# Performance work log

Measured on AMD Instinct MI355X. Metric: run time of the kernel, lower is better.

The kernel has to match this reference:

```python
import jax, jax.numpy as jnp
import numpy as np

N = 50000          # nodes
E = 1000000        # edges
EMB = 64           # emb_dim
L = 3              # num_layer
B = 250            # graphs (200 nodes each)
XF, EF = 7, 5      # node / edge feature dims
BN_EPS = 1e-5


def setup_inputs() -> dict:
    key = jax.random.key(0)
    ks = jax.random.split(key, 16)
    x = jax.random.normal(ks[0], (N, XF), dtype=jnp.float32)
    edge_attr = jax.random.normal(ks[1], (E, EF), dtype=jnp.float32)
    edge_index = jax.random.randint(ks[2], (2, E), 0, N, dtype=jnp.int32)
    # 250 contiguous graphs of 200 nodes: last node index of each graph
    last_idx = jnp.arange(1, B + 1, dtype=jnp.int32) * (N // B) - 1
    s = 0.05
    xW = jax.random.normal(ks[3], (XF, EMB), dtype=jnp.float32) * s
    xb = jnp.zeros((EMB,), dtype=jnp.float32)
    eW = jax.random.normal(ks[4], (L, EF, EMB), dtype=jnp.float32) * s
    eb = jnp.zeros((L, EMB), dtype=jnp.float32)
    W1 = jax.random.normal(ks[5], (L, EMB, 2 * EMB), dtype=jnp.float32) * s
    b1 = jnp.zeros((L, 2 * EMB), dtype=jnp.float32)
    W2 = jax.random.normal(ks[6], (L, 2 * EMB, EMB), dtype=jnp.float32) * s
    b2 = jnp.zeros((L, EMB), dtype=jnp.float32)
    gamma = jnp.ones((L, EMB), dtype=jnp.float32)
    beta = jnp.zeros((L, EMB), dtype=jnp.float32)
    return {"x": x, "edge_attr": edge_attr, "edge_index": edge_index,
            "last_idx": last_idx, "xW": xW, "xb": xb, "eW": eW, "eb": eb,
            "W1": W1, "b1": b1, "W2": W2, "b2": b2,
            "gamma": gamma, "beta": beta}


def _gnn_forward(x, edge_attr, edge_index, last_idx, xW, xb, eW, eb, W1, b1, W2, b2, gamma, beta):
    n = x.shape[0]
    # self-loop edge attrs: first column = 8, rest 0
    self_attr = jnp.zeros((n, EF), dtype=edge_attr.dtype).at[:, 0].set(8.0)
    ea = jnp.concatenate([edge_attr, self_attr], axis=0)          # [E+N, EF]
    loop = jnp.arange(n, dtype=edge_index.dtype)
    src = jnp.concatenate([edge_index[0], loop])                  # x_j indices
    dst = jnp.concatenate([edge_index[1], loop])                  # aggregation targets

    h = x @ xW + xb                                               # [N, EMB]
    for l in range(L):
        e = ea @ eW[l] + eb[l]                                    # [E+N, EMB]
        msg = h[src] + e                                          # gather + combine
        agg = jax.ops.segment_sum(msg, dst, num_segments=n)       # scatter-add
        h2 = jax.nn.relu(agg @ W1[l] + b1[l]) @ W2[l] + b2[l]     # GIN MLP
        mean = jnp.mean(h2, axis=0)
        var = jnp.mean(jnp.square(h2 - mean), axis=0)             # biased, like torch BN
        hn = (h2 - mean) * jax.lax.rsqrt(var + BN_EPS) * gamma[l] + beta[l]
        h = jax.nn.elu(hn) if l < L - 1 else hn                   # drop_ratio = 0
    return h[last_idx]                                            # super-node reps [B, EMB]


def reference(x, edge_attr, edge_index, last_idx, xW, xb, eW, eb, W1, b1, W2, b2, gamma, beta):
    return _gnn_forward(x, edge_attr, edge_index, last_idx, xW, xb, eW, eb, W1, b1, W2, b2, gamma, beta)
```

## Files before the change

kernel.cpp:

```cpp
#include <hip/hip_runtime.h>

#define N_NODES 50000
#define N_EDGES 1000000
#define EMB     64
#define HID     128
#define NLAYER  3
#define NGRAPH  250
#define XFD     7
#define EFD     5
#define BN_EPS  1e-5f

#define NBKT  196
#define CHKE  4096
#define NCHK  245
#define CNTM  (NBKT * NCHK)
#define NB2   ((CNTM + 255) / 256)

__device__ __forceinline__ void atomAddF(float* p, float v) {
    __hip_atomic_fetch_add(p, v, __ATOMIC_RELAXED, __HIP_MEMORY_SCOPE_AGENT);
}

__global__ void k_input(const float* __restrict__ x, const float* __restrict__ xW,
                        const float* __restrict__ xb, float* __restrict__ h) {
    int gid = blockIdx.x * 256 + threadIdx.x;
    if (gid >= N_NODES * EMB) return;
    int n = gid >> 6, f = gid & 63;
    float acc = xb[f];
#pragma unroll
    for (int k = 0; k < XFD; ++k) acc = fmaf(x[n * XFD + k], xW[k * EMB + f], acc);
    h[gid] = acc;
}

__global__ __launch_bounds__(256) void k_binA(const int* __restrict__ dst,
                                              int* __restrict__ cntmat) {
    __shared__ int hist[NBKT];
    int tid = threadIdx.x, c = blockIdx.x;
    for (int i = tid; i < NBKT; i += 256) hist[i] = 0;
    __syncthreads();
    int e0 = c * CHKE, e1 = min(e0 + CHKE, N_EDGES);
    for (int i = e0 + tid; i < e1; i += 256) atomicAdd(&hist[dst[i] >> 8], 1);
    __syncthreads();
    for (int b = tid; b < NBKT; b += 256) cntmat[b * NCHK + c] = hist[b];
}

__global__ __launch_bounds__(256) void k_gscanA(const int* __restrict__ in, int n,
                                                int* __restrict__ bsum) {
    int tid = threadIdx.x, lane = tid & 63, wid = tid >> 6;
    int i = blockIdx.x * 256 + tid;
    int v = (i < n) ? in[i] : 0;
#pragma unroll
    for (int off = 32; off; off >>= 1) v += __shfl_down(v, off);
    __shared__ int ws[4];
    if (lane == 0) ws[wid] = v;
    __syncthreads();
    if (tid == 0) bsum[blockIdx.x] = ws[0] + ws[1] + ws[2] + ws[3];
}

__global__ __launch_bounds__(256) void k_gscanB(const int* __restrict__ bsum, int nb,
                                                int* __restrict__ boff) {
    int tid = threadIdx.x, lane = tid & 63, wid = tid >> 6;
    int v = (tid < nb) ? bsum[tid] : 0;
    int x = v;
#pragma unroll
    for (int off = 1; off < 64; off <<= 1) {
        int y = __shfl_up(x, off);
        if (lane >= off) x += y;
    }
    __shared__ int wtot[4];
    if (lane == 63) wtot[wid] = x;
    __syncthreads();
    int woff = 0;
    for (int w = 0; w < wid; ++w) woff += wtot[w];
    if (tid < nb) boff[tid] = woff + x - v;
}

__global__ __launch_bounds__(256) void k_gscanC(const int* __restrict__ in, int n,
                                                const int* __restrict__ boff,
                                                int* __restrict__ out) {
    int tid = threadIdx.x, lane = tid & 63, wid = tid >> 6;
    int i = blockIdx.x * 256 + tid;
    int v = (i < n) ? in[i] : 0;
    int x = v;
#pragma unroll
    for (int off = 1; off < 64; off <<= 1) {
        int y = __shfl_up(x, off);
        if (lane >= off) x += y;
    }
    __shared__ int wtot[4];
    if (lane == 63) wtot[wid] = x;
    __syncthreads();
    int woff = boff[blockIdx.x];
    for (int w = 0; w < wid; ++w) woff += wtot[w];
    if (i < n) out[i] = woff + x - v;
}

__global__ __launch_bounds__(256) void k_binC(const int* __restrict__ src,
                                              const int* __restrict__ dst,
                                              const int* __restrict__ off2,
                                              int4* __restrict__ buf) {
    __shared__ int cur[NBKT];
    int tid = threadIdx.x, c = blockIdx.x;
    for (int b = tid; b < NBKT; b += 256) cur[b] = off2[b * NCHK + c];
    __syncthreads();
    int e0 = c * CHKE, e1 = min(e0 + CHKE, N_EDGES);
    for (int i = e0 + tid; i < e1; i += 256) {
        int d = dst[i];
        int b = d >> 8;
        int p = atomicAdd(&cur[b], 1);
        buf[p] = make_int4(src[i], i, d, 0);
    }
}

__global__ __launch_bounds__(256) void k_binD(const int4* __restrict__ buf,
                                              const int* __restrict__ off2,
                                              const float* __restrict__ ea,
                                              int* __restrict__ csr,
                                              int* __restrict__ rowstart,
                                              float* __restrict__ aggE) {
    __shared__ int hist[256];
    __shared__ int cur[256];
    __shared__ float accL[256 * EFD];
    __shared__ int wtot[4];
    int tid = threadIdx.x, b = blockIdx.x;
    int bstart = off2[b * NCHK];
    int bend = (b + 1 < NBKT) ? off2[(b + 1) * NCHK] : N_EDGES;
    hist[tid] = 0;
    for (int i = tid; i < 256 * EFD; i += 256) accL[i] = 0.f;
    __syncthreads();
    for (int j = bstart + tid; j < bend; j += 256) atomicAdd(&hist[buf[j].z & 255], 1);
    __syncthreads();
    int lane = tid & 63, wid = tid >> 6;
    int v = hist[tid], x = v;
#pragma unroll
    for (int off = 1; off < 64; off <<= 1) {
        int y = __shfl_up(x, off);
        if (lane >= off) x += y;
    }
    if (lane == 63) wtot[wid] = x;
    __syncthreads();
    int woff = 0;
    for (int w = 0; w < wid; ++w) woff += wtot[w];
    int ex = woff + x - v;
    cur[tid] = ex;
    int node = b * 256 + tid;
    if (node < N_NODES) rowstart[node] = bstart + ex;
    if (b == NBKT - 1 && tid == 255) rowstart[N_NODES] = N_EDGES;
    __syncthreads();
    for (int j = bstart + tid; j < bend; j += 256) {
        int4 t = buf[j];
        int local = t.z & 255;
        int p = atomicAdd(&cur[local], 1);
        csr[bstart + p] = t.x;
        const float* pe = ea + (size_t)t.y * EFD;
        atomicAdd(&accL[local * EFD + 0], pe[0]);
        atomicAdd(&accL[local * EFD + 1], pe[1]);
        atomicAdd(&accL[local * EFD + 2], pe[2]);
        atomicAdd(&accL[local * EFD + 3], pe[3]);
        atomicAdd(&accL[local * EFD + 4], pe[4]);
    }
    __syncthreads();
    int validN = min(256, N_NODES - b * 256);
    for (int i = tid; i < validN * EFD; i += 256)
        aggE[(size_t)b * 256 * EFD + i] = accL[i];
}

__global__ __launch_bounds__(256) void k_agg(const float* __restrict__ h,
                                             float* __restrict__ agg,
                                             const int* __restrict__ rowstart,
                                             const int* __restrict__ csr,
                                             const float* __restrict__ aggE,
                                             const float* __restrict__ eWl,
                                             const float* __restrict__ ebl) {
    int wid = (blockIdx.x * 256 + threadIdx.x) >> 6;
    int lane = threadIdx.x & 63;
    if (wid >= N_NODES) return;
    int n = wid;
    int lg = lane >> 4, lq = lane & 15;
    const float4* h4 = (const float4*)h;
    int j0 = rowstart[n], j1 = rowstart[n + 1];
    float4 acc = make_float4(0.f, 0.f, 0.f, 0.f);
    int j = j0;
    while (j < j1) {
        int take = j1 - j;
        if (take > 64) take = 64;
        int myid = (lane < take) ? csr[j + lane] : 0;
        int nt = (take + 3) >> 2;
        int t = 0;
        for (; t + 4 <= nt; t += 4) {
            int e0 = t * 4 + lg, e1 = e0 + 4, e2 = e0 + 8, e3 = e0 + 12;
            int s0 = __shfl(myid, e0), s1 = __shfl(myid, e1),
                s2 = __shfl(myid, e2), s3 = __shfl(myid, e3);
            float4 v0 = h4[(size_t)s0 * 16 + lq];
            float4 v1 = h4[(size_t)s1 * 16 + lq];
            float4 v2 = h4[(size_t)s2 * 16 + lq];
            float4 v3 = h4[(size_t)s3 * 16 + lq];
            if (e0 < take) { acc.x += v0.x; acc.y += v0.y; acc.z += v0.z; acc.w += v0.w; }
            if (e1 < take) { acc.x += v1.x; acc.y += v1.y; acc.z += v1.z; acc.w += v1.w; }
            if (e2 < take) { acc.x += v2.x; acc.y += v2.y; acc.z += v2.z; acc.w += v2.w; }
            if (e3 < take) { acc.x += v3.x; acc.y += v3.y; acc.z += v3.z; acc.w += v3.w; }
        }
        for (; t < nt; ++t) {
            int e = t * 4 + lg;
            int s = __shfl(myid, e);
            float4 v = h4[(size_t)s * 16 + lq];
            if (e < take) { acc.x += v.x; acc.y += v.y; acc.z += v.z; acc.w += v.w; }
        }
        j += take;
    }
    acc.x += __shfl_xor(acc.x, 16); acc.y += __shfl_xor(acc.y, 16);
    acc.z += __shfl_xor(acc.z, 16); acc.w += __shfl_xor(acc.w, 16);
    acc.x += __shfl_xor(acc.x, 32); acc.y += __shfl_xor(acc.y, 32);
    acc.z += __shfl_xor(acc.z, 32); acc.w += __shfl_xor(acc.w, 32);
    const float4* eW4 = (const float4*)eWl;
    float4 ew0 = eW4[lq], ew1 = eW4[16 + lq], ew2 = eW4[32 + lq],
           ew3 = eW4[48 + lq], ew4 = eW4[64 + lq];
    float4 eb4 = ((const float4*)ebl)[lq];
    float a0 = aggE[n * 5 + 0], a1 = aggE[n * 5 + 1], a2 = aggE[n * 5 + 2],
          a3 = aggE[n * 5 + 3], a4 = aggE[n * 5 + 4];
    float c0 = a0 + 8.f;
    float ce = (float)(j1 - j0) + 1.f;
    float4 bb = h4[(size_t)n * 16 + lq];
    bb.x = fmaf(c0, ew0.x, bb.x); bb.y = fmaf(c0, ew0.y, bb.y);
    bb.z = fmaf(c0, ew0.z, bb.z); bb.w = fmaf(c0, ew0.w, bb.w);
    bb.x = fmaf(a1, ew1.x, bb.x); bb.y = fmaf(a1, ew1.y, bb.y);
    bb.z = fmaf(a1, ew1.z, bb.z); bb.w = fmaf(a1, ew1.w, bb.w);
    bb.x = fmaf(a2, ew2.x, bb.x); bb.y = fmaf(a2, ew2.y, bb.y);
    bb.z = fmaf(a2, ew2.z, bb.z); bb.w = fmaf(a2, ew2.w, bb.w);
    bb.x = fmaf(a3, ew3.x, bb.x); bb.y = fmaf(a3, ew3.y, bb.y);
    bb.z = fmaf(a3, ew3.z, bb.z); bb.w = fmaf(a3, ew3.w, bb.w);
    bb.x = fmaf(a4, ew4.x, bb.x); bb.y = fmaf(a4, ew4.y, bb.y);
    bb.z = fmaf(a4, ew4.z, bb.z); bb.w = fmaf(a4, ew4.w, bb.w);
    bb.x = fmaf(ce, eb4.x, bb.x); bb.y = fmaf(ce, eb4.y, bb.y);
    bb.z = fmaf(ce, eb4.z, bb.z); bb.w = fmaf(ce, eb4.w, bb.w);
    if (lg == 0) {
        ((float4*)agg)[(size_t)n * 16 + lq] =
            make_float4(acc.x + bb.x, acc.y + bb.y, acc.z + bb.z, acc.w + bb.w);
    }
}

__global__ __launch_bounds__(256) void k_mlp1(const float* __restrict__ agg,
                                              float* __restrict__ hidden,
                                              const float* __restrict__ W1l,
                                              const float* __restrict__ b1l) {
    __shared__ float w1s[64 * 128];
    __shared__ float as[32 * 68];
    __shared__ float b1s[128];
    int tid = threadIdx.x;
    int n0 = blockIdx.x * 32;
    const float4* wg = (const float4*)W1l;
    float4* wsh = (float4*)w1s;
#pragma unroll
    for (int i = 0; i < 8; ++i) wsh[tid + i * 256] = wg[tid + i * 256];
    if (tid < 128) b1s[tid] = b1l[tid];
    const float4* ag4 = (const float4*)agg;
#pragma unroll
    for (int i = 0; i < 2; ++i) {
        int idx = tid + i * 256;
        int m = idx >> 4, kq = idx & 15;
        int nn = n0 + m;
        float4 v = make_float4(0.f, 0.f, 0.f, 0.f);
        if (nn < N_NODES) v = ag4[nn * 16 + kq];
        *(float4*)&as[m * 68 + kq * 4] = v;
    }
    __syncthreads();
    int j0 = (tid & 31) * 4;
    int m0 = (tid >> 5) * 4;
    float acc[4][4] = {};
#pragma unroll 8
    for (int k = 0; k < 64; ++k) {
        float4 w = *(const float4*)&w1s[k * 128 + j0];
        float a0 = as[(m0 + 0) * 68 + k];
        float a1 = as[(m0 + 1) * 68 + k];
        float a2 = as[(m0 + 2) * 68 + k];
        float a3 = as[(m0 + 3) * 68 + k];
        acc[0][0] = fmaf(a0, w.x, acc[0][0]); acc[0][1] = fmaf(a0, w.y, acc[0][1]);
        acc[0][2] = fmaf(a0, w.z, acc[0][2]); acc[0][3] = fmaf(a0, w.w, acc[0][3]);
        acc[1][0] = fmaf(a1, w.x, acc[1][0]); acc[1][1] = fmaf(a1, w.y, acc[1][1]);
        acc[1][2] = fmaf(a1, w.z, acc[1][2]); acc[1][3] = fmaf(a1, w.w, acc[1][3]);
        acc[2][0] = fmaf(a2, w.x, acc[2][0]); acc[2][1] = fmaf(a2, w.y, acc[2][1]);
        acc[2][2] = fmaf(a2, w.z, acc[2][2]); acc[2][3] = fmaf(a2, w.w, acc[2][3]);
        acc[3][0] = fmaf(a3, w.x, acc[3][0]); acc[3][1] = fmaf(a3, w.y, acc[3][1]);
        acc[3][2] = fmaf(a3, w.z, acc[3][2]); acc[3][3] = fmaf(a3, w.w, acc[3][3]);
    }
#pragma unroll
    for (int a = 0; a < 4; ++a) {
        int nn = n0 + m0 + a;
        if (nn < N_NODES) {
            float4 o;
            o.x = fmaxf(acc[a][0] + b1s[j0 + 0], 0.f);
            o.y = fmaxf(acc[a][1] + b1s[j0 + 1], 0.f);
            o.z = fmaxf(acc[a][2] + b1s[j0 + 2], 0.f);
            o.w = fmaxf(acc[a][3] + b1s[j0 + 3], 0.f);
            *(float4*)&hidden[nn * HID + j0] = o;
        }
    }
}

__global__ __launch_bounds__(256) void k_mlp2(const float* __restrict__ hidden,
                                              float* __restrict__ h2,
                                              const float* __restrict__ W2l,
                                              const float* __restrict__ b2l,
                                              float* __restrict__ stats) {
    __shared__ float w2s[128 * 64];
    __shared__ float hs[64 * 132];
    __shared__ float b2s[64];
    int tid = threadIdx.x;
    int n0 = blockIdx.x * 64;
    const float4* wg = (const float4*)W2l;
    float4* wsh = (float4*)w2s;
#pragma unroll
    for (int i = 0; i < 8; ++i) wsh[tid + i * 256] = wg[tid + i * 256];
    if (tid < 64) b2s[tid] = b2l[tid];
    const float4* hg4 = (const float4*)hidden;
#pragma unroll
    for (int i = 0; i < 8; ++i) {
        int idx = tid + i * 256;
        int m = idx >> 5, kq = idx & 31;
        int nn = n0 + m;
        float4 v = make_float4(0.f, 0.f, 0.f, 0.f);
        if (nn < N_NODES) v = hg4[nn * 32 + kq];
        *(float4*)&hs[m * 132 + kq * 4] = v;
    }
    __syncthreads();
    int f0 = (tid & 15) * 4;
    int m0 = (tid >> 4) * 4;
    float acc[4][4] = {};
#pragma unroll 8
    for (int k = 0; k < 128; ++k) {
        float4 w = *(const float4*)&w2s[k * 64 + f0];
        float a0 = hs[(m0 + 0) * 132 + k];
        float a1 = hs[(m0 + 1) * 132 + k];
        float a2 = hs[(m0 + 2) * 132 + k];
        float a3 = hs[(m0 + 3) * 132 + k];
        acc[0][0] = fmaf(a0, w.x, acc[0][0]); acc[0][1] = fmaf(a0, w.y, acc[0][1]);
        acc[0][2] = fmaf(a0, w.z, acc[0][2]); acc[0][3] = fmaf(a0, w.w, acc[0][3]);
        acc[1][0] = fmaf(a1, w.x, acc[1][0]); acc[1][1] = fmaf(a1, w.y, acc[1][1]);
        acc[1][2] = fmaf(a1, w.z, acc[1][2]); acc[1][3] = fmaf(a1, w.w, acc[1][3]);
        acc[2][0] = fmaf(a2, w.x, acc[2][0]); acc[2][1] = fmaf(a2, w.y, acc[2][1]);
        acc[2][2] = fmaf(a2, w.z, acc[2][2]); acc[2][3] = fmaf(a2, w.w, acc[2][3]);
        acc[3][0] = fmaf(a3, w.x, acc[3][0]); acc[3][1] = fmaf(a3, w.y, acc[3][1]);
        acc[3][2] = fmaf(a3, w.z, acc[3][2]); acc[3][3] = fmaf(a3, w.w, acc[3][3]);
    }
    float sf[4] = {0.f, 0.f, 0.f, 0.f}, qf[4] = {0.f, 0.f, 0.f, 0.f};
#pragma unroll
    for (int a = 0; a < 4; ++a) {
        int nn = n0 + m0 + a;
        if (nn < N_NODES) {
            float v0 = acc[a][0] + b2s[f0 + 0];
            float v1 = acc[a][1] + b2s[f0 + 1];
            float v2 = acc[a][2] + b2s[f0 + 2];
            float v3 = acc[a][3] + b2s[f0 + 3];
            *(float4*)&h2[nn * EMB + f0] = make_float4(v0, v1, v2, v3);
            sf[0] += v0; sf[1] += v1; sf[2] += v2; sf[3] += v3;
            qf[0] = fmaf(v0, v0, qf[0]); qf[1] = fmaf(v1, v1, qf[1]);
            qf[2] = fmaf(v2, v2, qf[2]); qf[3] = fmaf(v3, v3, qf[3]);
        }
    }
    __syncthreads();
    float* red = hs;
    int mg = tid >> 4;
#pragma unroll
    for (int j = 0; j < 4; ++j) {
        red[mg * 64 + f0 + j] = sf[j];
        red[1024 + mg * 64 + f0 + j] = qf[j];
    }
    __syncthreads();
    if (tid < 64) {
        float s = 0.f, q = 0.f;
#pragma unroll
        for (int m = 0; m < 16; ++m) {
            s += red[m * 64 + tid];
            q += red[1024 + m * 64 + tid];
        }
        atomAddF(&stats[tid], s);
        atomAddF(&stats[64 + tid], q);
    }
}

__global__ void k_bn(const float* __restrict__ h2, float* __restrict__ h,
                     const float* __restrict__ stats, const float* __restrict__ gam,
                     const float* __restrict__ bet) {
    int gid = blockIdx.x * 256 + threadIdx.x;
    if (gid >= N_NODES * EMB) return;
    int f = gid & 63;
    const float invN = 1.f / (float)N_NODES;
    float mean = stats[f] * invN;
    float var = stats[64 + f] * invN - mean * mean;
    float inv = rsqrtf(var + BN_EPS);
    float v = (h2[gid] - mean) * inv * gam[f] + bet[f];
    h[gid] = v > 0.f ? v : expm1f(v);
}

__global__ void k_bnout(const float* __restrict__ h2, const int* __restrict__ last,
                        const float* __restrict__ stats, const float* __restrict__ gam,
                        const float* __restrict__ bet, float* __restrict__ out) {
    int gid = blockIdx.x * 256 + threadIdx.x;
    if (gid >= NGRAPH * EMB) return;
    int b = gid >> 6, f = gid & 63;
    const float invN = 1.f / (float)N_NODES;
    float mean = stats[f] * invN;
    float var = stats[64 + f] * invN - mean * mean;
    float inv = rsqrtf(var + BN_EPS);
    out[gid] = (h2[last[b] * EMB + f] - mean) * inv * gam[f] + bet[f];
}

extern "C" void kernel_launch(void* const* d_in, const int* in_sizes, int n_in,
                              void* d_out, int out_size, void* d_ws, size_t ws_size,
                              hipStream_t stream) {
    const float* x   = (const float*)d_in[0];
    const float* ea  = (const float*)d_in[1];
    const int*   eidx= (const int*)d_in[2];
    const int*   last= (const int*)d_in[3];
    const float* xW  = (const float*)d_in[4];
    const float* xb  = (const float*)d_in[5];
    const float* eW  = (const float*)d_in[6];
    const float* eb  = (const float*)d_in[7];
    const float* W1  = (const float*)d_in[8];
    const float* b1  = (const float*)d_in[9];
    const float* W2  = (const float*)d_in[10];
    const float* b2  = (const float*)d_in[11];
    const float* gam = (const float*)d_in[12];
    const float* bet = (const float*)d_in[13];
    float* out = (float*)d_out;

    const int* srcI = eidx;
    const int* dstI = eidx + N_EDGES;

    float* h      = (float*)d_ws;
    float* agg    = h + N_NODES * EMB;
    float* hidden = agg + N_NODES * EMB;
    float* aggE   = hidden + N_NODES * HID;
    float* stats  = aggE + N_NODES * EFD;
    int* rowstart = (int*)(stats + NLAYER * 2 * EMB);
    int* csr      = rowstart + N_NODES + 1;
    int* cntmat   = csr + N_EDGES;
    int* off2     = cntmat + CNTM;
    int* bsum     = off2 + CNTM;
    int* boff     = bsum + NB2;
    int4* buf     = (int4*)hidden;

    hipMemsetAsync(stats, 0, NLAYER * 2 * EMB * sizeof(float), stream);

    k_input<<<(N_NODES * EMB + 255) / 256, 256, 0, stream>>>(x, xW, xb, h);
    k_binA<<<NCHK, 256, 0, stream>>>(dstI, cntmat);
    k_gscanA<<<NB2, 256, 0, stream>>>(cntmat, CNTM, bsum);
    k_gscanB<<<1, 256, 0, stream>>>(bsum, NB2, boff);
    k_gscanC<<<NB2, 256, 0, stream>>>(cntmat, CNTM, boff, off2);
    k_binC<<<NCHK, 256, 0, stream>>>(srcI, dstI, off2, buf);
    k_binD<<<NBKT, 256, 0, stream>>>(buf, off2, ea, csr, rowstart, aggE);

    for (int l = 0; l < NLAYER; ++l) {
        k_agg<<<(N_NODES * 64 + 255) / 256, 256, 0, stream>>>(
            h, agg, rowstart, csr, aggE, eW + l * EFD * EMB, eb + l * EMB);
        k_mlp1<<<(N_NODES + 31) / 32, 256, 0, stream>>>(agg, hidden, W1 + l * EMB * HID,
                                                        b1 + l * HID);
        k_mlp2<<<(N_NODES + 63) / 64, 256, 0, stream>>>(hidden, agg, W2 + l * HID * EMB,
                                                        b2 + l * EMB, stats + l * 2 * EMB);
        if (l < NLAYER - 1) {
            k_bn<<<(N_NODES * EMB + 255) / 256, 256, 0, stream>>>(
                agg, h, stats + l * 2 * EMB, gam + l * EMB, bet + l * EMB);
        } else {
            k_bnout<<<(NGRAPH * EMB + 255) / 256, 256, 0, stream>>>(
                agg, last, stats + l * 2 * EMB, gam + l * EMB, bet + l * EMB, out);
        }
    }
}
```

Measured before the change: 430.4 us.

## Halve bucket size and move edge-attr gather into binning pass

Shrinks the destination buckets from 256 to 128 nodes, doubling the number of k_binD blocks so the per-bucket pass spreads over more CUs, and enlarges the global scan to 512 threads to cover the larger count matrix. k_binC now reads each edge's attributes in edge order (coalesced) and writes them next to the binned src/local-dst pairs in split SoA buffers. k_binD then reads them contiguously instead of gathering by edge id. The binned staging data gets larger and is written to more buffers, in exchange for removing the random gather over edge_attr.

New measurement: 452.5 us. 1.05x slower.

```diff
diff --git a/kernel.cpp b/kernel.cpp
--- a/kernel.cpp
+++ b/kernel.cpp
@@ -10,11 +10,13 @@
 #define EFD     5
 #define BN_EPS  1e-5f
 
-#define NBKT  196
-#define CHKE  4096
-#define NCHK  245
-#define CNTM  (NBKT * NCHK)
-#define NB2   ((CNTM + 255) / 256)
+#define BKT_SH 7
+#define BKT_SZ 128
+#define NBKT   ((N_NODES + BKT_SZ - 1) / BKT_SZ)
+#define CHKE   4096
+#define NCHK   ((N_EDGES + CHKE - 1) / CHKE)
+#define CNTM   (NBKT * NCHK)
+#define NB2    ((CNTM + 255) / 256)
 
 __device__ __forceinline__ void atomAddF(float* p, float v) {
     __hip_atomic_fetch_add(p, v, __ATOMIC_RELAXED, __HIP_MEMORY_SCOPE_AGENT);
@@ -38,7 +40,7 @@
     for (int i = tid; i < NBKT; i += 256) hist[i] = 0;
     __syncthreads();
     int e0 = c * CHKE, e1 = min(e0 + CHKE, N_EDGES);
-    for (int i = e0 + tid; i < e1; i += 256) atomicAdd(&hist[dst[i] >> 8], 1);
+    for (int i = e0 + tid; i < e1; i += 256) atomicAdd(&hist[dst[i] >> BKT_SH], 1);
     __syncthreads();
     for (int b = tid; b < NBKT; b += 256) cntmat[b * NCHK + c] = hist[b];
 }
@@ -56,7 +58,7 @@
     if (tid == 0) bsum[blockIdx.x] = ws[0] + ws[1] + ws[2] + ws[3];
 }
 
-__global__ __launch_bounds__(256) void k_gscanB(const int* __restrict__ bsum, int nb,
+__global__ __launch_bounds__(512) void k_gscanB(const int* __restrict__ bsum, int nb,
                                                 int* __restrict__ boff) {
     int tid = threadIdx.x, lane = tid & 63, wid = tid >> 6;
     int v = (tid < nb) ? bsum[tid] : 0;
@@ -66,7 +68,7 @@
         int y = __shfl_up(x, off);
         if (lane >= off) x += y;
     }
-    __shared__ int wtot[4];
+    __shared__ int wtot[8];
     if (lane == 63) wtot[wid] = x;
     __syncthreads();
     int woff = 0;
@@ -96,8 +98,11 @@
 
 __global__ __launch_bounds__(256) void k_binC(const int* __restrict__ src,
                                               const int* __restrict__ dst,
+                                              const float* __restrict__ ea,
                                               const int* __restrict__ off2,
-                                              int4* __restrict__ buf) {
+                                              int2* __restrict__ bufSD,
+                                              float4* __restrict__ bufEA,
+                                              float* __restrict__ bufE4) {
     __shared__ int cur[NBKT];
     int tid = threadIdx.x, c = blockIdx.x;
     for (int b = tid; b < NBKT; b += 256) cur[b] = off2[b * NCHK + c];
@@ -105,32 +110,36 @@
     int e0 = c * CHKE, e1 = min(e0 + CHKE, N_EDGES);
     for (int i = e0 + tid; i < e1; i += 256) {
         int d = dst[i];
-        int b = d >> 8;
+        int b = d >> BKT_SH;
         int p = atomicAdd(&cur[b], 1);
-        buf[p] = make_int4(src[i], i, d, 0);
-    }
-}
-
-__global__ __launch_bounds__(256) void k_binD(const int4* __restrict__ buf,
+        const float* pe = ea + (size_t)i * EFD;
+        bufSD[p] = make_int2(src[i], d & (BKT_SZ - 1));
+        bufEA[p] = make_float4(pe[0], pe[1], pe[2], pe[3]);
+        bufE4[p] = pe[4];
+    }
+}
+
+__global__ __launch_bounds__(256) void k_binD(const int2* __restrict__ bufSD,
+                                              const float4* __restrict__ bufEA,
+                                              const float* __restrict__ bufE4,
                                               const int* __restrict__ off2,
-                                              const float* __restrict__ ea,
                                               int* __restrict__ csr,
                                               int* __restrict__ rowstart,
                                               float* __restrict__ aggE) {
-    __shared__ int hist[256];
-    __shared__ int cur[256];
-    __shared__ float accL[256 * EFD];
+    __shared__ int hist[BKT_SZ];
+    __shared__ int cur[BKT_SZ];
+    __shared__ float accL[BKT_SZ * EFD];
     __shared__ int wtot[4];
     int tid = threadIdx.x, b = blockIdx.x;
     int bstart = off2[b * NCHK];
     int bend = (b + 1 < NBKT) ? off2[(b + 1) * NCHK] : N_EDGES;
-    hist[tid] = 0;
-    for (int i = tid; i < 256 * EFD; i += 256) accL[i] = 0.f;
-    __syncthreads();
-    for (int j = bstart + tid; j < bend; j += 256) atomicAdd(&hist[buf[j].z & 255], 1);
+    if (tid < BKT_SZ) hist[tid] = 0;
+    for (int i = tid; i < BKT_SZ * EFD; i += 256) accL[i] = 0.f;
+    __syncthreads();
+    for (int j = bstart + tid; j < bend; j += 256) atomicAdd(&hist[bufSD[j].y], 1);
     __syncthreads();
     int lane = tid & 63, wid = tid >> 6;
-    int v = hist[tid], x = v;
+    int v = (tid < BKT_SZ) ? hist[tid] : 0, x = v;
 #pragma unroll
     for (int off = 1; off < 64; off <<= 1) {
         int y = __shfl_up(x, off);
@@ -141,27 +150,30 @@
     int woff = 0;
     for (int w = 0; w < wid; ++w) woff += wtot[w];
     int ex = woff + x - v;
-    cur[tid] = ex;
-    int node = b * 256 + tid;
-    if (node < N_NODES) rowstart[node] = bstart + ex;
-    if (b == NBKT - 1 && tid == 255) rowstart[N_NODES] = N_EDGES;
+    if (tid < BKT_SZ) {
+        cur[tid] = ex;
+        int node = b * BKT_SZ + tid;
+        if (node < N_NODES) rowstart[node] = bstart + ex;
+    }
+    if (b == NBKT - 1 && tid == 0) rowstart[N_NODES] = N_EDGES;
     __syncthreads();
     for (int j = bstart + tid; j < bend; j += 256) {
-        int4 t = buf[j];
-        int local = t.z & 255;
-        int p = atomicAdd(&cur[local], 1);
+        int2 t = bufSD[j];
+        float4 f4 = bufEA[j];
+        float f1 = bufE4[j];
+        int p = atomicAdd(&cur[t.y], 1);
         csr[bstart + p] = t.x;
-        const float* pe = ea + (size_t)t.y * EFD;
-        atomicAdd(&accL[local * EFD + 0], pe[0]);
-        atomicAdd(&accL[local * EFD + 1], pe[1]);
-        atomicAdd(&accL[local * EFD + 2], pe[2]);
-        atomicAdd(&accL[local * EFD + 3], pe[3]);
-        atomicAdd(&accL[local * EFD + 4], pe[4]);
-    }
-    __syncthreads();
-    int validN = min(256, N_NODES - b * 256);
+        float* a = accL + t.y * EFD;
+        atomicAdd(&a[0], f4.x);
+        atomicAdd(&a[1], f4.y);
+        atomicAdd(&a[2], f4.z);
+        atomicAdd(&a[3], f4.w);
+        atomicAdd(&a[4], f1);
+    }
+    __syncthreads();
+    int validN = min(BKT_SZ, N_NODES - b * BKT_SZ);
     for (int i = tid; i < validN * EFD; i += 256)
-        aggE[(size_t)b * 256 * EFD + i] = accL[i];
+        aggE[(size_t)b * BKT_SZ * EFD + i] = accL[i];
 }
 
 __global__ __launch_bounds__(256) void k_agg(const float* __restrict__ h,
@@ -430,24 +442,26 @@
     float* agg    = h + N_NODES * EMB;
     float* hidden = agg + N_NODES * EMB;
     float* aggE   = hidden + N_NODES * HID;
-    float* stats  = aggE + N_NODES * EFD;
+    float* stats  = aggE + NBKT * BKT_SZ * EFD;
     int* rowstart = (int*)(stats + NLAYER * 2 * EMB);
     int* csr      = rowstart + N_NODES + 1;
     int* cntmat   = csr + N_EDGES;
     int* off2     = cntmat + CNTM;
     int* bsum     = off2 + CNTM;
     int* boff     = bsum + NB2;
-    int4* buf     = (int4*)hidden;
+    int2*   bufSD = (int2*)agg;
+    float4* bufEA = (float4*)hidden;
+    float*  bufE4 = (float*)(hidden + N_EDGES * 4);
 
     hipMemsetAsync(stats, 0, NLAYER * 2 * EMB * sizeof(float), stream);
 
     k_input<<<(N_NODES * EMB + 255) / 256, 256, 0, stream>>>(x, xW, xb, h);
     k_binA<<<NCHK, 256, 0, stream>>>(dstI, cntmat);
     k_gscanA<<<NB2, 256, 0, stream>>>(cntmat, CNTM, bsum);
-    k_gscanB<<<1, 256, 0, stream>>>(bsum, NB2, boff);
+    k_gscanB<<<1, 512, 0, stream>>>(bsum, NB2, boff);
     k_gscanC<<<NB2, 256, 0, stream>>>(cntmat, CNTM, boff, off2);
-    k_binC<<<NCHK, 256, 0, stream>>>(srcI, dstI, off2, buf);
-    k_binD<<<NBKT, 256, 0, stream>>>(buf, off2, ea, csr, rowstart, aggE);
+    k_binC<<<NCHK, 256, 0, stream>>>(srcI, dstI, ea, off2, bufSD, bufEA, bufE4);
+    k_binD<<<NBKT, 256, 0, stream>>>(bufSD, bufEA, bufE4, off2, csr, rowstart, aggE);
 
     for (int l = 0; l < NLAYER; ++l) {
         k_agg<<<(N_NODES * 64 + 255) / 256, 256, 0, stream>>>(
```
